# Kernel tuning notes

Hardware: AMD Instinct MI355X
Metric: run time of the kernel (lower is better)

## Reference

```python
import jax, jax.numpy as jnp
import numpy as np

NUM_CLASSES = 1000
FEAT_DIM = 512
BATCH = 16384


def setup_inputs() -> dict:
    key = jax.random.key(0)
    k1, k2, k3 = jax.random.split(key, 3)
    x = jax.random.normal(k1, (BATCH, FEAT_DIM), dtype=jnp.float32)
    labels = jax.random.randint(k2, (BATCH,), 0, NUM_CLASSES, dtype=jnp.int64)
    centers = jax.random.normal(k3, (NUM_CLASSES, FEAT_DIM), dtype=jnp.float32)
    margin = jnp.ones((1,), dtype=jnp.float32)
    return {"x": x, "labels": labels, "centers": centers, "margin": margin}


def reference(x, labels, centers, margin):
    # squared euclidean distances: [B, C]
    distmat = (
        jnp.sum(x * x, axis=1, keepdims=True)
        + jnp.sum(centers * centers, axis=1)[None, :]
        - 2.0 * (x @ centers.T)
    )
    B, C = distmat.shape
    onehot = labels[:, None] == jnp.arange(C, dtype=labels.dtype)[None, :]  # [B, C]
    # distance to the true-class center
    dist = jnp.sum(jnp.where(onehot, distmat, 0.0), axis=1)  # [B]
    # min distance over all other classes (mask true class with +inf)
    dist_min = jnp.min(jnp.where(onehot, jnp.inf, distmat), axis=1)  # [B]
    m = margin[0]
    loss = jnp.sum(jnp.maximum(m + dist - dist_min, 0.0)) / B
    return loss
```

## Files before the change

### kernel.cpp

```cpp
#include <hip/hip_runtime.h>
#include <hip/hip_bf16.h>

#define BATCH 16384
#define NCLS  1000
#define NPAD  1024
#define FDIM  512

#define CBLK_STRIDE 266240
#define TAIL_OFF    262144

typedef __bf16 bf16x4 __attribute__((ext_vector_type(4)));
typedef __bf16 bf16x8 __attribute__((ext_vector_type(8)));
typedef float  f32x16 __attribute__((ext_vector_type(16)));

#define GLOBAL_AS __attribute__((address_space(1)))
#define LDS_AS    __attribute__((address_space(3)))

#define VMCNT(n) asm volatile("s_waitcnt vmcnt(" #n ")" ::: "memory")
#define LGKM0()  asm volatile("s_waitcnt lgkmcnt(0)" ::: "memory")
#define BAR()    do { LGKM0(); __builtin_amdgcn_s_barrier(); \
                      __builtin_amdgcn_sched_barrier(0); } while (0)

__global__ __launch_bounds__(64) void prep_centers(
    const float* __restrict__ centers, char* __restrict__ cbt)
{
    const int c = blockIdx.x, t = threadIdx.x;
    const int cblk = c >> 8, cl = c & 255;
    char* base = cbt + (size_t)cblk * CBLK_STRIDE;

    float4 f0 = make_float4(0.f, 0.f, 0.f, 0.f);
    float4 f1 = make_float4(0.f, 0.f, 0.f, 0.f);
    if (c < NCLS) {
        f0 = *(const float4*)(centers + (size_t)c * FDIM + t * 8);
        f1 = *(const float4*)(centers + (size_t)c * FDIM + t * 8 + 4);
    }
    bf16x8 b;
    b[0] = (__bf16)f0.x; b[1] = (__bf16)f0.y; b[2] = (__bf16)f0.z; b[3] = (__bf16)f0.w;
    b[4] = (__bf16)f1.x; b[5] = (__bf16)f1.y; b[6] = (__bf16)f1.z; b[7] = (__bf16)f1.w;
    *(bf16x8*)(base + (t >> 2) * 16384 + (t & 3) * 4096 + cl * 16) = b;

    float ssum = f0.x*f0.x + f0.y*f0.y + f0.z*f0.z + f0.w*f0.w
               + f1.x*f1.x + f1.y*f1.y + f1.z*f1.z + f1.w*f1.w;
    #pragma unroll
    for (int o = 32; o > 0; o >>= 1) ssum += __shfl_down(ssum, o);
    if (t == 0) {
        const float hf = (c < NCLS) ? (-0.5f * ssum) : -1e30f;
        const __bf16 h = (__bf16)hf;
        const __bf16 l = (c < NCLS) ? (__bf16)(hf - (float)h) : (__bf16)0.f;
        bf16x8 tl;
        #pragma unroll
        for (int e = 0; e < 8; ++e) tl[e] = (__bf16)0.f;
        tl[0] = h; tl[1] = l;
        *(bf16x8*)(base + TAIL_OFF + cl * 16) = tl;
    }
}

struct B4 { float4 a, b, c, d; };

__global__ __launch_bounds__(256, 2) void trip_main(
    const float* __restrict__ x, const int* __restrict__ labels,
    const char* __restrict__ cbt, float* __restrict__ mxp,
    float* __restrict__ dap)
{
    extern __shared__ char lds[];
    const int t    = threadIdx.x;
    const int lane = t & 63;
    const int w    = t >> 6;
    const int wN   = w & 1, wM = w >> 1;
    const int l31  = lane & 31, hi = lane >> 5;
    const int bid  = blockIdx.x;
    const int cblk = bid >> 7;
    const int bblk = bid & 127;
    const int class0 = cblk * 256;
    const int row0   = bblk * 128;
    const char* cbB  = cbt + (size_t)cblk * CBLK_STRIDE;

    auto stageA = [&](int ko, int ai) {
        const char* src = cbB + ko * 16384 + w * 4096 + lane * 16;
        char* dst = lds + ai * 16384 + w * 4096 + lane * 16;
        #pragma unroll
        for (int j = 0; j < 4; ++j)
            __builtin_amdgcn_global_load_lds(
                (const GLOBAL_AS void*)(src + j * 1024),
                (LDS_AS void*)(dst + j * 1024), 16, 0, 0);
    };
    auto loadB = [&](int ko, B4& br) {
        const float* src = x + (size_t)row0 * FDIM + ko * 32
                         + (size_t)(w * 32 + (lane >> 3)) * FDIM + (lane & 7) * 4;
        br.a = *(const float4*)(src);
        br.b = *(const float4*)(src +  8 * FDIM);
        br.c = *(const float4*)(src + 16 * FDIM);
        br.d = *(const float4*)(src + 24 * FDIM);
    };
    auto cv4 = [](float4 f) {
        bf16x4 v;
        v[0] = (__bf16)f.x; v[1] = (__bf16)f.y;
        v[2] = (__bf16)f.z; v[3] = (__bf16)f.w;
        return v;
    };
    auto writeB = [&](const B4& br, int bi) {
        char* dst = lds + 49152 + bi * 8192 + ((lane & 7) >> 1) * 2048
                  + (w * 32 + (lane >> 3)) * 16 + (lane & 1) * 8;
        *(bf16x4*)(dst      ) = cv4(br.a);
        *(bf16x4*)(dst + 128) = cv4(br.b);
        *(bf16x4*)(dst + 256) = cv4(br.c);
        *(bf16x4*)(dst + 384) = cv4(br.d);
    };

    f32x16 acc[4][2];
    #pragma unroll
    for (int mi = 0; mi < 4; ++mi)
        #pragma unroll
        for (int ni = 0; ni < 2; ++ni)
            #pragma unroll
            for (int r = 0; r < 16; ++r) acc[mi][ni][r] = 0.f;

    auto compute = [&](int buf) {
        const char* A = lds + buf * 16384;
        const char* B = lds + 49152 + buf * 8192;
        #pragma unroll
        for (int ks = 0; ks < 2; ++ks) {
            const int chunk = ks * 2 + hi;
            bf16x8 a[4], b[2];
            #pragma unroll
            for (int mi = 0; mi < 4; ++mi)
                a[mi] = *(const bf16x8*)(A + chunk * 4096 + (wM * 128 + mi * 32 + l31) * 16);
            #pragma unroll
            for (int ni = 0; ni < 2; ++ni)
                b[ni] = *(const bf16x8*)(B + chunk * 2048 + (wN * 64 + ni * 32 + l31) * 16);
            #pragma unroll
            for (int mi = 0; mi < 4; ++mi)
                #pragma unroll
                for (int ni = 0; ni < 2; ++ni)
                    acc[mi][ni] = __builtin_amdgcn_mfma_f32_32x32x16_bf16(
                        a[mi], b[ni], acc[mi][ni], 0, 0, 0);
        }
    };

    const int lab0 = labels[row0 + wN * 64 + l31];
    const int lab1 = labels[row0 + wN * 64 + 32 + l31];
    {
        const char* src = cbB + TAIL_OFF + t * 16;
        char* dst = lds + 73728 + t * 16;
        __builtin_amdgcn_global_load_lds((const GLOBAL_AS void*)src,
                                         (LDS_AS void*)dst, 16, 0, 0);
    }
    B4 brA, brB;
    stageA(0, 0); loadB(0, brA);
    __builtin_amdgcn_sched_barrier(0);
    stageA(1, 1); loadB(1, brB);
    VMCNT(8);
    writeB(brA, 0);
    BAR();

    #pragma unroll
    for (int tt = 0; tt < 16; ++tt) {
        const int cur = tt % 3, wr = (tt + 1) % 3, pre = (tt + 2) % 3;
        if (tt < 14) {
            stageA(tt + 2, pre);
            if (tt & 1) loadB(tt + 2, brB);
            else        loadB(tt + 2, brA);
            VMCNT(8);
        } else {
            VMCNT(0);
        }
        if (tt < 15) {
            if (tt & 1) writeB(brA, wr);
            else        writeB(brB, wr);
        }
        compute(cur);
        BAR();
    }

    {
        const char* T = lds + 73728;
        bf16x8 bt;
        #pragma unroll
        for (int e = 0; e < 8; ++e) bt[e] = (__bf16)0.f;
        if (hi == 0) { bt[0] = (__bf16)1.0f; bt[1] = (__bf16)1.0f; }
        #pragma unroll
        for (int mi = 0; mi < 4; ++mi) {
            bf16x8 a = *(const bf16x8*)(T + (wM * 128 + mi * 32 + l31) * 16);
            #pragma unroll
            for (int ni = 0; ni < 2; ++ni)
                acc[mi][ni] = __builtin_amdgcn_mfma_f32_32x32x16_bf16(
                    a, bt, acc[mi][ni], 0, 0, 0);
        }
    }

    const int labBase = class0 + wM * 128 + hi * 4;
    const int labA0 = lab0 - labBase;
    const int labA1 = lab1 - labBase;
    float MX0 = -3e38f, MX1 = -3e38f, DA0 = -3e38f, DA1 = -3e38f;
    #pragma unroll
    for (int mi = 0; mi < 4; ++mi) {
        #pragma unroll
        for (int r = 0; r < 16; ++r) {
            const int pat = mi * 32 + (r & 3) + 8 * (r >> 2);
            {
                const float a = acc[mi][0][r];
                const bool is = (labA0 == pat);
                MX0 = fmaxf(MX0, is ? -3e38f : a);
                DA0 = is ? a : DA0;
            }
            {
                const float a = acc[mi][1][r];
                const bool is = (labA1 == pat);
                MX1 = fmaxf(MX1, is ? -3e38f : a);
                DA1 = is ? a : DA1;
            }
        }
    }
    MX0 = fmaxf(MX0, __shfl_xor(MX0, 32));
    DA0 = fmaxf(DA0, __shfl_xor(DA0, 32));
    MX1 = fmaxf(MX1, __shfl_xor(MX1, 32));
    DA1 = fmaxf(DA1, __shfl_xor(DA1, 32));

    float* sc = (float*)lds;
    const int i0 = wN * 64 + l31;
    const int i1 = i0 + 32;
    if (wM == 1 && hi == 0) {
        sc[i0] = MX0; sc[128 + i0] = DA0;
        sc[i1] = MX1; sc[128 + i1] = DA1;
    }
    __syncthreads();
    if (wM == 0 && hi == 0) {
        const float M0 = fmaxf(MX0, sc[i0]),  D0 = fmaxf(DA0, sc[128 + i0]);
        const float M1 = fmaxf(MX1, sc[i1]),  D1 = fmaxf(DA1, sc[128 + i1]);
        const int rg = row0 + wN * 64 + l31;
        mxp[cblk * BATCH + rg]      = M0;
        dap[cblk * BATCH + rg]      = D0;
        mxp[cblk * BATCH + rg + 32] = M1;
        dap[cblk * BATCH + rg + 32] = D1;
    }
}

__global__ __launch_bounds__(256) void combine1(
    const float* __restrict__ mxp, const float* __restrict__ dap,
    const float* __restrict__ margin, float* __restrict__ partial)
{
    const int t = threadIdx.x;
    const int row = blockIdx.x * 256 + t;
    float mx = mxp[row];
    mx = fmaxf(mx, mxp[BATCH + row]);
    mx = fmaxf(mx, mxp[2 * BATCH + row]);
    mx = fmaxf(mx, mxp[3 * BATCH + row]);
    float da = dap[row];
    da = fmaxf(da, dap[BATCH + row]);
    da = fmaxf(da, dap[2 * BATCH + row]);
    da = fmaxf(da, dap[3 * BATCH + row]);
    float loss = fmaxf(margin[0] - 2.f * da + 2.f * mx, 0.f);
    __shared__ float red[4];
    #pragma unroll
    for (int o = 32; o > 0; o >>= 1) loss += __shfl_down(loss, o);
    if ((t & 63) == 0) red[t >> 6] = loss;
    __syncthreads();
    if (t == 0) partial[blockIdx.x] = red[0] + red[1] + red[2] + red[3];
}

__global__ __launch_bounds__(64) void combine2(
    const float* __restrict__ partial, float* __restrict__ out)
{
    float s = partial[threadIdx.x];
    #pragma unroll
    for (int o = 32; o > 0; o >>= 1) s += __shfl_down(s, o);
    if (threadIdx.x == 0) out[0] = s * (1.0f / BATCH);
}

extern "C" void kernel_launch(void* const* d_in, const int* in_sizes, int n_in,
                              void* d_out, int out_size, void* d_ws, size_t ws_size,
                              hipStream_t stream)
{
    const float* x       = (const float*)d_in[0];
    const int*   labels  = (const int*)d_in[1];
    const float* centers = (const float*)d_in[2];
    const float* margin  = (const float*)d_in[3];
    float* out = (float*)d_out;

    char* ws = (char*)d_ws;
    char*  cbt  = ws;
    float* mxp  = (float*)(ws + 1064960);
    float* dap  = (float*)(ws + 1327104);
    float* part = (float*)(ws + 1589248);

    (void)hipFuncSetAttribute((const void*)trip_main,
                              hipFuncAttributeMaxDynamicSharedMemorySize, 77824);

    prep_centers<<<NPAD, 64, 0, stream>>>(centers, cbt);
    trip_main<<<512, 256, 77824, stream>>>(x, labels, cbt, mxp, dap);
    combine1<<<64, 256, 0, stream>>>(mxp, dap, margin, part);
    combine2<<<1, 64, 0, stream>>>(part, out);
}
```

Before: 33.46 us.

## Double batch tile per block to 256 rows and fuse final reduction via atomics

Each main-kernel block now covers 256 batch rows instead of 128, so the number of blocks halves to 256. Each wave holds a 4x4 grid of MFMA accumulators, and each staged centers tile is reused across twice as many rows. The two-stage final reduction is folded into one kernel that atomically adds into the output, which prep_centers now zeroes, removing one launch. The cost is more registers and LDS, with occupancy dropping to one block per CU, and 256 blocks may not fill all CUs on the device.

```diff
diff --git a/kernel.cpp b/kernel.cpp
--- a/kernel.cpp
+++ b/kernel.cpp
@@ -22,11 +22,13 @@
                       __builtin_amdgcn_sched_barrier(0); } while (0)
 
 __global__ __launch_bounds__(64) void prep_centers(
-    const float* __restrict__ centers, char* __restrict__ cbt)
+    const float* __restrict__ centers, char* __restrict__ cbt,
+    float* __restrict__ out)
 {
     const int c = blockIdx.x, t = threadIdx.x;
     const int cblk = c >> 8, cl = c & 255;
     char* base = cbt + (size_t)cblk * CBLK_STRIDE;
+    if (c == 0 && t == 0) out[0] = 0.f;
 
     float4 f0 = make_float4(0.f, 0.f, 0.f, 0.f);
     float4 f1 = make_float4(0.f, 0.f, 0.f, 0.f);
@@ -55,9 +57,9 @@
     }
 }
 
-struct B4 { float4 a, b, c, d; };
-
-__global__ __launch_bounds__(256, 2) void trip_main(
+struct B8 { float4 a, b, c, d, e, f, g, h; };
+
+__global__ __launch_bounds__(256, 1) void trip_main(
     const float* __restrict__ x, const int* __restrict__ labels,
     const char* __restrict__ cbt, float* __restrict__ mxp,
     float* __restrict__ dap)
@@ -69,10 +71,10 @@
     const int wN   = w & 1, wM = w >> 1;
     const int l31  = lane & 31, hi = lane >> 5;
     const int bid  = blockIdx.x;
-    const int cblk = bid >> 7;
-    const int bblk = bid & 127;
+    const int cblk = bid >> 6;
+    const int bblk = bid & 63;
     const int class0 = cblk * 256;
-    const int row0   = bblk * 128;
+    const int row0   = bblk * 256;
     const char* cbB  = cbt + (size_t)cblk * CBLK_STRIDE;
 
     auto stageA = [&](int ko, int ai) {
@@ -84,13 +86,17 @@
                 (const GLOBAL_AS void*)(src + j * 1024),
                 (LDS_AS void*)(dst + j * 1024), 16, 0, 0);
     };
-    auto loadB = [&](int ko, B4& br) {
+    auto loadB = [&](int ko, B8& br) {
         const float* src = x + (size_t)row0 * FDIM + ko * 32
-                         + (size_t)(w * 32 + (lane >> 3)) * FDIM + (lane & 7) * 4;
+                         + (size_t)(w * 64 + (lane >> 3)) * FDIM + (lane & 7) * 4;
         br.a = *(const float4*)(src);
         br.b = *(const float4*)(src +  8 * FDIM);
         br.c = *(const float4*)(src + 16 * FDIM);
         br.d = *(const float4*)(src + 24 * FDIM);
+        br.e = *(const float4*)(src + 32 * FDIM);
+        br.f = *(const float4*)(src + 40 * FDIM);
+        br.g = *(const float4*)(src + 48 * FDIM);
+        br.h = *(const float4*)(src + 56 * FDIM);
     };
     auto cv4 = [](float4 f) {
         bf16x4 v;
@@ -98,58 +104,64 @@
         v[2] = (__bf16)f.z; v[3] = (__bf16)f.w;
         return v;
     };
-    auto writeB = [&](const B4& br, int bi) {
-        char* dst = lds + 49152 + bi * 8192 + ((lane & 7) >> 1) * 2048
-                  + (w * 32 + (lane >> 3)) * 16 + (lane & 1) * 8;
+    auto writeB = [&](const B8& br, int bi) {
+        char* dst = lds + 49152 + bi * 16384 + ((lane & 7) >> 1) * 4096
+                  + (w * 64 + (lane >> 3)) * 16 + (lane & 1) * 8;
         *(bf16x4*)(dst      ) = cv4(br.a);
         *(bf16x4*)(dst + 128) = cv4(br.b);
         *(bf16x4*)(dst + 256) = cv4(br.c);
         *(bf16x4*)(dst + 384) = cv4(br.d);
-    };
-
-    f32x16 acc[4][2];
+        *(bf16x4*)(dst + 512) = cv4(br.e);
+        *(bf16x4*)(dst + 640) = cv4(br.f);
+        *(bf16x4*)(dst + 768) = cv4(br.g);
+        *(bf16x4*)(dst + 896) = cv4(br.h);
+    };
+
+    f32x16 acc[4][4];
     #pragma unroll
     for (int mi = 0; mi < 4; ++mi)
         #pragma unroll
-        for (int ni = 0; ni < 2; ++ni)
+        for (int ni = 0; ni < 4; ++ni)
             #pragma unroll
             for (int r = 0; r < 16; ++r) acc[mi][ni][r] = 0.f;
 
     auto compute = [&](int buf) {
         const char* A = lds + buf * 16384;
-        const char* B = lds + 49152 + buf * 8192;
+        const char* B = lds + 49152 + buf * 16384;
         #pragma unroll
         for (int ks = 0; ks < 2; ++ks) {
             const int chunk = ks * 2 + hi;
-            bf16x8 a[4], b[2];
+            bf16x8 a[4], b[4];
             #pragma unroll
             for (int mi = 0; mi < 4; ++mi)
                 a[mi] = *(const bf16x8*)(A + chunk * 4096 + (wM * 128 + mi * 32 + l31) * 16);
             #pragma unroll
-            for (int ni = 0; ni < 2; ++ni)
-                b[ni] = *(const bf16x8*)(B + chunk * 2048 + (wN * 64 + ni * 32 + l31) * 16);
+            for (int ni = 0; ni < 4; ++ni)
+                b[ni] = *(const bf16x8*)(B + chunk * 4096 + (wN * 128 + ni * 32 + l31) * 16);
             #pragma unroll
             for (int mi = 0; mi < 4; ++mi)
                 #pragma unroll
-                for (int ni = 0; ni < 2; ++ni)
+                for (int ni = 0; ni < 4; ++ni)
                     acc[mi][ni] = __builtin_amdgcn_mfma_f32_32x32x16_bf16(
                         a[mi], b[ni], acc[mi][ni], 0, 0, 0);
         }
     };
 
-    const int lab0 = labels[row0 + wN * 64 + l31];
-    const int lab1 = labels[row0 + wN * 64 + 32 + l31];
+    const int lab0 = labels[row0 + wN * 128 +  0 + l31];
+    const int lab1 = labels[row0 + wN * 128 + 32 + l31];
+    const int lab2 = labels[row0 + wN * 128 + 64 + l31];
+    const int lab3 = labels[row0 + wN * 128 + 96 + l31];
     {
         const char* src = cbB + TAIL_OFF + t * 16;
-        char* dst = lds + 73728 + t * 16;
+        char* dst = lds + 98304 + t * 16;
         __builtin_amdgcn_global_load_lds((const GLOBAL_AS void*)src,
                                          (LDS_AS void*)dst, 16, 0, 0);
     }
-    B4 brA, brB;
+    B8 brA, brB;
     stageA(0, 0); loadB(0, brA);
     __builtin_amdgcn_sched_barrier(0);
     stageA(1, 1); loadB(1, brB);
-    VMCNT(8);
+    VMCNT(12);
     writeB(brA, 0);
     BAR();
 
@@ -160,7 +172,7 @@
             stageA(tt + 2, pre);
             if (tt & 1) loadB(tt + 2, brB);
             else        loadB(tt + 2, brA);
-            VMCNT(8);
+            VMCNT(12);
         } else {
             VMCNT(0);
         }
@@ -173,7 +185,7 @@
     }
 
     {
-        const char* T = lds + 73728;
+        const char* T = lds + 98304;
         bf16x8 bt;
         #pragma unroll
         for (int e = 0; e < 8; ++e) bt[e] = (__bf16)0.f;
@@ -182,89 +194,80 @@
         for (int mi = 0; mi < 4; ++mi) {
             bf16x8 a = *(const bf16x8*)(T + (wM * 128 + mi * 32 + l31) * 16);
             #pragma unroll
-            for (int ni = 0; ni < 2; ++ni)
+            for (int ni = 0; ni < 4; ++ni)
                 acc[mi][ni] = __builtin_amdgcn_mfma_f32_32x32x16_bf16(
                     a, bt, acc[mi][ni], 0, 0, 0);
         }
     }
 
     const int labBase = class0 + wM * 128 + hi * 4;
-    const int labA0 = lab0 - labBase;
-    const int labA1 = lab1 - labBase;
-    float MX0 = -3e38f, MX1 = -3e38f, DA0 = -3e38f, DA1 = -3e38f;
+    const int lA0 = lab0 - labBase, lA1 = lab1 - labBase;
+    const int lA2 = lab2 - labBase, lA3 = lab3 - labBase;
+    float MX0 = -3e38f, MX1 = -3e38f, MX2 = -3e38f, MX3 = -3e38f;
+    float DA0 = -3e38f, DA1 = -3e38f, DA2 = -3e38f, DA3 = -3e38f;
     #pragma unroll
     for (int mi = 0; mi < 4; ++mi) {
         #pragma unroll
         for (int r = 0; r < 16; ++r) {
             const int pat = mi * 32 + (r & 3) + 8 * (r >> 2);
-            {
-                const float a = acc[mi][0][r];
-                const bool is = (labA0 == pat);
-                MX0 = fmaxf(MX0, is ? -3e38f : a);
-                DA0 = is ? a : DA0;
-            }
-            {
-                const float a = acc[mi][1][r];
-                const bool is = (labA1 == pat);
-                MX1 = fmaxf(MX1, is ? -3e38f : a);
-                DA1 = is ? a : DA1;
-            }
-        }
-    }
-    MX0 = fmaxf(MX0, __shfl_xor(MX0, 32));
-    DA0 = fmaxf(DA0, __shfl_xor(DA0, 32));
-    MX1 = fmaxf(MX1, __shfl_xor(MX1, 32));
-    DA1 = fmaxf(DA1, __shfl_xor(DA1, 32));
+            { const float a = acc[mi][0][r]; const bool is = (lA0 == pat);
+              MX0 = fmaxf(MX0, is ? -3e38f : a); DA0 = is ? a : DA0; }
+            { const float a = acc[mi][1][r]; const bool is = (lA1 == pat);
+              MX1 = fmaxf(MX1, is ? -3e38f : a); DA1 = is ? a : DA1; }
+            { const float a = acc[mi][2][r]; const bool is = (lA2 == pat);
+              MX2 = fmaxf(MX2, is ? -3e38f : a); DA2 = is ? a : DA2; }
+            { const float a = acc[mi][3][r]; const bool is = (lA3 == pat);
+              MX3 = fmaxf(MX3, is ? -3e38f : a); DA3 = is ? a : DA3; }
+        }
+    }
+    MX0 = fmaxf(MX0, __shfl_xor(MX0, 32)); DA0 = fmaxf(DA0, __shfl_xor(DA0, 32));
+    MX1 = fmaxf(MX1, __shfl_xor(MX1, 32)); DA1 = fmaxf(DA1, __shfl_xor(DA1, 32));
+    MX2 = fmaxf(MX2, __shfl_xor(MX2, 32)); DA2 = fmaxf(DA2, __shfl_xor(DA2, 32));
+    MX3 = fmaxf(MX3, __shfl_xor(MX3, 32)); DA3 = fmaxf(DA3, __shfl_xor(DA3, 32));
 
     float* sc = (float*)lds;
-    const int i0 = wN * 64 + l31;
-    const int i1 = i0 + 32;
+    const int i0 = wN * 128 +  0 + l31;
+    const int i1 = wN * 128 + 32 + l31;
+    const int i2 = wN * 128 + 64 + l31;
+    const int i3 = wN * 128 + 96 + l31;
     if (wM == 1 && hi == 0) {
-        sc[i0] = MX0; sc[128 + i0] = DA0;
-        sc[i1] = MX1; sc[128 + i1] = DA1;
+        sc[i0] = MX0; sc[256 + i0] = DA0;
+        sc[i1] = MX1; sc[256 + i1] = DA1;
+        sc[i2] = MX2; sc[256 + i2] = DA2;
+        sc[i3] = MX3; sc[256 + i3] = DA3;
     }
     __syncthreads();
     if (wM == 0 && hi == 0) {
-        const float M0 = fmaxf(MX0, sc[i0]),  D0 = fmaxf(DA0, sc[128 + i0]);
-        const float M1 = fmaxf(MX1, sc[i1]),  D1 = fmaxf(DA1, sc[128 + i1]);
-        const int rg = row0 + wN * 64 + l31;
-        mxp[cblk * BATCH + rg]      = M0;
-        dap[cblk * BATCH + rg]      = D0;
-        mxp[cblk * BATCH + rg + 32] = M1;
-        dap[cblk * BATCH + rg + 32] = D1;
-    }
-}
-
-__global__ __launch_bounds__(256) void combine1(
+        const int rg = row0 + wN * 128 + l31;
+        mxp[cblk * BATCH + rg     ] = fmaxf(MX0, sc[i0]);
+        dap[cblk * BATCH + rg     ] = fmaxf(DA0, sc[256 + i0]);
+        mxp[cblk * BATCH + rg + 32] = fmaxf(MX1, sc[i1]);
+        dap[cblk * BATCH + rg + 32] = fmaxf(DA1, sc[256 + i1]);
+        mxp[cblk * BATCH + rg + 64] = fmaxf(MX2, sc[i2]);
+        dap[cblk * BATCH + rg + 64] = fmaxf(DA2, sc[256 + i2]);
+        mxp[cblk * BATCH + rg + 96] = fmaxf(MX3, sc[i3]);
+        dap[cblk * BATCH + rg + 96] = fmaxf(DA3, sc[256 + i3]);
+    }
+}
+
+__global__ __launch_bounds__(256) void combine(
     const float* __restrict__ mxp, const float* __restrict__ dap,
-    const float* __restrict__ margin, float* __restrict__ partial)
+    const float* __restrict__ margin, float* __restrict__ out)
 {
     const int t = threadIdx.x;
     const int row = blockIdx.x * 256 + t;
-    float mx = mxp[row];
-    mx = fmaxf(mx, mxp[BATCH + row]);
-    mx = fmaxf(mx, mxp[2 * BATCH + row]);
-    mx = fmaxf(mx, mxp[3 * BATCH + row]);
-    float da = dap[row];
-    da = fmaxf(da, dap[BATCH + row]);
-    da = fmaxf(da, dap[2 * BATCH + row]);
-    da = fmaxf(da, dap[3 * BATCH + row]);
+    float mx = fmaxf(fmaxf(mxp[row], mxp[BATCH + row]),
+                     fmaxf(mxp[2 * BATCH + row], mxp[3 * BATCH + row]));
+    float da = fmaxf(fmaxf(dap[row], dap[BATCH + row]),
+                     fmaxf(dap[2 * BATCH + row], dap[3 * BATCH + row]));
     float loss = fmaxf(margin[0] - 2.f * da + 2.f * mx, 0.f);
     __shared__ float red[4];
     #pragma unroll
     for (int o = 32; o > 0; o >>= 1) loss += __shfl_down(loss, o);
     if ((t & 63) == 0) red[t >> 6] = loss;
     __syncthreads();
-    if (t == 0) partial[blockIdx.x] = red[0] + red[1] + red[2] + red[3];
-}
-
-__global__ __launch_bounds__(64) void combine2(
-    const float* __restrict__ partial, float* __restrict__ out)
-{
-    float s = partial[threadIdx.x];
-    #pragma unroll
-    for (int o = 32; o > 0; o >>= 1) s += __shfl_down(s, o);
-    if (threadIdx.x == 0) out[0] = s * (1.0f / BATCH);
+    if (t == 0)
+        atomicAdd(out, (red[0] + red[1] + red[2] + red[3]) * (1.0f / BATCH));
 }
 
 extern "C" void kernel_launch(void* const* d_in, const int* in_sizes, int n_in,
@@ -281,13 +284,11 @@
     char*  cbt  = ws;
     float* mxp  = (float*)(ws + 1064960);
     float* dap  = (float*)(ws + 1327104);
-    float* part = (float*)(ws + 1589248);
 
     (void)hipFuncSetAttribute((const void*)trip_main,
-                              hipFuncAttributeMaxDynamicSharedMemorySize, 77824);
-
-    prep_centers<<<NPAD, 64, 0, stream>>>(centers, cbt);
-    trip_main<<<512, 256, 77824, stream>>>(x, labels, cbt, mxp, dap);
-    combine1<<<64, 256, 0, stream>>>(mxp, dap, margin, part);
-    combine2<<<1, 64, 0, stream>>>(part, out);
-}
+                              hipFuncAttributeMaxDynamicSharedMemorySize, 102400);
+
+    prep_centers<<<NPAD, 64, 0, stream>>>(centers, cbt, out);
+    trip_main<<<256, 256, 102400, stream>>>(x, labels, cbt, mxp, dap);
+    combine<<<64, 256, 0, stream>>>(mxp, dap, margin, out);
+}
```

Result: slower. 36.63 us (+9.5%).
